# Kernel tuning notes

Hardware: AMD Instinct MI355X
Metric: run time of the kernel (lower is better)

The kernel has to match this reference:

```python
import jax, jax.numpy as jnp
import numpy as np

NUM_BASES = 8


def setup_inputs() -> dict:
    key = jax.random.key(0)
    ks = jax.random.split(key, 8)
    N, E = 100000, 1600000
    IN_F, OUT_F, NUM_RELS = 128, 128, 16
    si = IN_F // NUM_BASES   # 16
    so = OUT_F // NUM_BASES  # 16
    return {
        "h": jax.random.normal(ks[0], (N, IN_F), dtype=jnp.float32),
        "norm": jax.random.uniform(ks[1], (N, 1), dtype=jnp.float32),
        "edge_src": jax.random.randint(ks[2], (E,), 0, N, dtype=jnp.int32),
        "edge_dst": jax.random.randint(ks[3], (E,), 0, N, dtype=jnp.int32),
        "edge_type": jax.random.randint(ks[4], (E,), 0, NUM_RELS, dtype=jnp.int32),
        "weight": jax.random.normal(ks[5], (NUM_RELS, NUM_BASES * si * so), dtype=jnp.float32) * 0.1,
        "bias_param": jax.random.normal(ks[6], (OUT_F,), dtype=jnp.float32) * 0.1,
        "loop_weight": jax.random.normal(ks[7], (IN_F, OUT_F), dtype=jnp.float32) * 0.1,
    }


def reference(h, norm, edge_src, edge_dst, edge_type, weight, bias_param, loop_weight):
    N, in_feat = h.shape
    out_feat = loop_weight.shape[1]
    si = in_feat // NUM_BASES
    so = out_feat // NUM_BASES
    E = edge_type.shape[0]

    # self-loop message (dropout=0.0 -> identity)
    loop_message = h @ loop_weight                      # [N, out_feat]

    # msg_func: gather per-edge relation weight blocks and do block-diag bmm
    W = weight[edge_type].reshape(E, NUM_BASES, si, so)  # [E, B, si, so]
    src = h[edge_src].reshape(E, NUM_BASES, si)          # [E, B, si]
    msg = jnp.einsum("ebi,ebio->ebo", src, W).reshape(E, out_feat)

    # scatter-sum messages to destination nodes, rescale by norm
    agg = jax.ops.segment_sum(msg, edge_dst, num_segments=N)  # [N, out_feat]
    node_repr = agg * norm

    # bias + self-loop + activation
    node_repr = node_repr + bias_param + loop_message
    return jax.nn.relu(node_repr)
```

## Files before the change

kernel.cpp:

```cpp
#include <hip/hip_runtime.h>


__device__ __forceinline__ unsigned int f2bf(float f) {
  const unsigned int u = __float_as_uint(f);
  return (u + 0x7FFFu + ((u >> 16) & 1u)) >> 16;
}

__global__ __launch_bounds__(256) void rgcn_init_kernel(
    const float* __restrict__ h, const float* __restrict__ loop_w,
    const float* __restrict__ bias, float* __restrict__ out, int N) {
  __shared__ float lw[128 * 128];
  for (int idx = threadIdx.x; idx < 128 * 128 / 4; idx += 256) {
    ((float4*)lw)[idx] = ((const float4*)loop_w)[idx];
  }
  __syncthreads();

  const int lane = threadIdx.x & 63;
  const int wid = threadIdx.x >> 6;
  const int group0 = blockIdx.x * 4 + wid;
  const int ngroups = gridDim.x * 4;
  const int totgroups = (N + 3) >> 2;
  const float b0 = bias[lane];
  const float b1 = bias[64 + lane];

  for (int g = group0; g < totgroups; g += ngroups) {
    const int n0 = g * 4;
    const int nn = (N - n0 < 4) ? (N - n0) : 4;
    if (nn == 4) {
      const float* __restrict__ r0 = h + (size_t)n0 * 128;
      const float* __restrict__ r1 = r0 + 128;
      const float* __restrict__ r2 = r1 + 128;
      const float* __restrict__ r3 = r2 + 128;
      float a00 = b0, a01 = b1, a10 = b0, a11 = b1;
      float a20 = b0, a21 = b1, a30 = b0, a31 = b1;
#pragma unroll 4
      for (int k = 0; k < 128; ++k) {
        const float w0 = lw[k * 128 + lane];
        const float w1 = lw[k * 128 + 64 + lane];
        a00 = fmaf(r0[k], w0, a00); a01 = fmaf(r0[k], w1, a01);
        a10 = fmaf(r1[k], w0, a10); a11 = fmaf(r1[k], w1, a11);
        a20 = fmaf(r2[k], w0, a20); a21 = fmaf(r2[k], w1, a21);
        a30 = fmaf(r3[k], w0, a30); a31 = fmaf(r3[k], w1, a31);
      }
      float* __restrict__ o0 = out + (size_t)n0 * 128;
      o0[lane] = a00;        o0[64 + lane] = a01;
      o0[128 + lane] = a10;  o0[192 + lane] = a11;
      o0[256 + lane] = a20;  o0[320 + lane] = a21;
      o0[384 + lane] = a30;  o0[448 + lane] = a31;
    } else {
      for (int r = 0; r < nn; ++r) {
        const int n = n0 + r;
        const float* __restrict__ hr = h + (size_t)n * 128;
        float a0 = b0, a1 = b1;
#pragma unroll 4
        for (int k = 0; k < 128; ++k) {
          const float a = hr[k];
          a0 = fmaf(a, lw[k * 128 + lane], a0);
          a1 = fmaf(a, lw[k * 128 + 64 + lane], a1);
        }
        out[(size_t)n * 128 + lane] = a0;
        out[(size_t)n * 128 + 64 + lane] = a1;
      }
    }
  }
}

__global__ __launch_bounds__(256) void rgcn_presence_kernel(
    const int* __restrict__ esrc, const int* __restrict__ etype,
    unsigned int* __restrict__ pres, int E) {
  for (int e = blockIdx.x * 256 + threadIdx.x; e < E; e += gridDim.x * 256)
    atomicOr(&pres[esrc[e]], 1u << etype[e]);
}

__global__ __launch_bounds__(1024, 8) void rgcn_precompute_kernel(
    const float* __restrict__ h, const float* __restrict__ weight,
    const unsigned int* __restrict__ pres, unsigned int* __restrict__ M,
    int base, int cend) {
  const int lane = threadIdx.x & 63;
  const int t = threadIdx.x >> 6;
  const int b = lane >> 4;
  const int o = lane & 15;

  const float* __restrict__ wb = weight + t * 2048 + b * 256 + o;
  float wlo[16], whi[16];
#pragma unroll
  for (int i = 0; i < 16; ++i) {
    wlo[i] = wb[i * 16];
    whi[i] = wb[1024 + i * 16];
  }

  const int span = cend - base;
  const int n0 = base + (int)(((long)blockIdx.x * span) / gridDim.x);
  const int n1 = base + (int)(((long)(blockIdx.x + 1) * span) / gridDim.x);

#pragma unroll 2
  for (int n = n0; n < n1; ++n) {
    if (!((pres[n] >> t) & 1u)) continue;

    const float4* __restrict__ hp =
        (const float4*)(h + (size_t)n * 128) + (b << 2);
    const float4 x0 = hp[0], x1 = hp[1], x2 = hp[2], x3 = hp[3];
    const float4 y0 = hp[16], y1 = hp[17], y2 = hp[18], y3 = hp[19];

    float a0 = x0.x * wlo[0], a1 = x0.y * wlo[1];
    a0 = fmaf(x0.z, wlo[2], a0);  a1 = fmaf(x0.w, wlo[3], a1);
    a0 = fmaf(x1.x, wlo[4], a0);  a1 = fmaf(x1.y, wlo[5], a1);
    a0 = fmaf(x1.z, wlo[6], a0);  a1 = fmaf(x1.w, wlo[7], a1);
    a0 = fmaf(x2.x, wlo[8], a0);  a1 = fmaf(x2.y, wlo[9], a1);
    a0 = fmaf(x2.z, wlo[10], a0); a1 = fmaf(x2.w, wlo[11], a1);
    a0 = fmaf(x3.x, wlo[12], a0); a1 = fmaf(x3.y, wlo[13], a1);
    a0 = fmaf(x3.z, wlo[14], a0); a1 = fmaf(x3.w, wlo[15], a1);

    float c0 = y0.x * whi[0], c1 = y0.y * whi[1];
    c0 = fmaf(y0.z, whi[2], c0);  c1 = fmaf(y0.w, whi[3], c1);
    c0 = fmaf(y1.x, whi[4], c0);  c1 = fmaf(y1.y, whi[5], c1);
    c0 = fmaf(y1.z, whi[6], c0);  c1 = fmaf(y1.w, whi[7], c1);
    c0 = fmaf(y2.x, whi[8], c0);  c1 = fmaf(y2.y, whi[9], c1);
    c0 = fmaf(y2.z, whi[10], c0); c1 = fmaf(y2.w, whi[11], c1);
    c0 = fmaf(y3.x, whi[12], c0); c1 = fmaf(y3.y, whi[13], c1);
    c0 = fmaf(y3.z, whi[14], c0); c1 = fmaf(y3.w, whi[15], c1);

    const unsigned int pk = f2bf(a0 + a1) | (f2bf(c0 + c1) << 16);
    M[(((size_t)(n - base) << 4) | t) * 64 + lane] = pk;
  }
}

__global__ __launch_bounds__(256) void rgcn_zero_kernel(int* __restrict__ p,
                                                        int n) {
  for (int i = blockIdx.x * 256 + threadIdx.x; i < n; i += gridDim.x * 256)
    p[i] = 0;
}

__global__ __launch_bounds__(256) void rgcn_hist_kernel(
    const int* __restrict__ esrc, const int* __restrict__ edst,
    int* __restrict__ cnt, int E, int N, unsigned S) {
  for (int e = blockIdx.x * 256 + threadIdx.x; e < E; e += gridDim.x * 256) {
    const unsigned q = (unsigned)esrc[e] / S;
    atomicAdd(&cnt[(int)(q * (unsigned)N) + edst[e]], 1);
  }
}

__global__ __launch_bounds__(1024) void rgcn_scan_pass1(
    const int* __restrict__ cnt, int* __restrict__ partial, int bins) {
  __shared__ int sums[1024];
  const int t = threadIdx.x;
  const int base = blockIdx.x * 4096 + t * 4;
  int s = 0;
  if (base + 3 < bins) {
    const int4 v = *(const int4*)(cnt + base);
    s = v.x + v.y + v.z + v.w;
  } else {
    for (int j = 0; j < 4; ++j)
      if (base + j < bins) s += cnt[base + j];
  }
  sums[t] = s;
  __syncthreads();
  for (int off = 512; off > 0; off >>= 1) {
    if (t < off) sums[t] += sums[t + off];
    __syncthreads();
  }
  if (t == 0) partial[blockIdx.x] = sums[0];
}

__global__ __launch_bounds__(1024) void rgcn_scan_pass2(
    int* __restrict__ partial, int nb) {
  __shared__ int sc[1024];
  const int t = threadIdx.x;
  int v[4];
  int s = 0;
#pragma unroll
  for (int j = 0; j < 4; ++j) {
    const int i = t * 4 + j;
    v[j] = (i < nb) ? partial[i] : 0;
    s += v[j];
  }
  sc[t] = s;
  __syncthreads();
#pragma unroll
  for (int off = 1; off < 1024; off <<= 1) {
    const int add = (t >= off) ? sc[t - off] : 0;
    __syncthreads();
    sc[t] += add;
    __syncthreads();
  }
  int run = (t == 0) ? 0 : sc[t - 1];
#pragma unroll
  for (int j = 0; j < 4; ++j) {
    const int i = t * 4 + j;
    if (i < nb) partial[i] = run;
    run += v[j];
  }
}

__global__ __launch_bounds__(1024) void rgcn_scan_pass3(
    const int* __restrict__ cnt, const int* __restrict__ partial,
    int* __restrict__ row_ptr, int* __restrict__ cursor, int bins) {
  __shared__ int sums[1024];
  const int t = threadIdx.x;
  const int base = blockIdx.x * 4096 + t * 4;
  int v0 = 0, v1 = 0, v2 = 0, v3 = 0;
  if (base + 3 < bins) {
    const int4 v = *(const int4*)(cnt + base);
    v0 = v.x; v1 = v.y; v2 = v.z; v3 = v.w;
  } else {
    if (base < bins) v0 = cnt[base];
    if (base + 1 < bins) v1 = cnt[base + 1];
    if (base + 2 < bins) v2 = cnt[base + 2];
  }
  sums[t] = v0 + v1 + v2 + v3;
  __syncthreads();
#pragma unroll
  for (int off = 1; off < 1024; off <<= 1) {
    const int add = (t >= off) ? sums[t - off] : 0;
    __syncthreads();
    sums[t] += add;
    __syncthreads();
  }
  const int run = partial[blockIdx.x] + ((t == 0) ? 0 : sums[t - 1]);
  const int p0 = run, p1 = p0 + v0, p2 = p1 + v1, p3 = p2 + v2;
  if (base + 3 < bins) {
    *(int4*)(row_ptr + base) = make_int4(p0, p1, p2, p3);
    *(int4*)(cursor + base) = make_int4(p0, p1, p2, p3);
  } else {
    if (base < bins) { row_ptr[base] = p0; cursor[base] = p0; }
    if (base + 1 < bins) { row_ptr[base + 1] = p1; cursor[base + 1] = p1; }
    if (base + 2 < bins) { row_ptr[base + 2] = p2; cursor[base + 2] = p2; }
  }
}

__global__ void rgcn_set_kernel(int* __restrict__ p, int v) {
  if (threadIdx.x == 0) *p = v;
}

__global__ __launch_bounds__(256) void rgcn_scatter_kernel(
    const int* __restrict__ esrc, const int* __restrict__ edst,
    const int* __restrict__ etype, int* __restrict__ cursor,
    int* __restrict__ srec, int E, int N, unsigned S) {
  for (int e = blockIdx.x * 256 + threadIdx.x; e < E; e += gridDim.x * 256) {
    const unsigned s = (unsigned)esrc[e];
    const unsigned q = s / S;
    const int key = (int)(q * (unsigned)N) + edst[e];
    const int p = atomicAdd(&cursor[key], 1);
    srec[p] = (int)((s - q * S) << 4) | etype[e];
  }
}

__global__ __launch_bounds__(256) void rgcn_gather3_kernel(
    const float* __restrict__ norm, const int* __restrict__ srec,
    const int* __restrict__ rpc, const unsigned int* __restrict__ M,
    float* __restrict__ out, int N, int final_pass) {
  const int lane = threadIdx.x & 63;
  const int w0 = blockIdx.x * 4 + (threadIdx.x >> 6);
  const int nw = gridDim.x * 4;

  for (int d = w0; d < N; d += nw) {
    const int e0 = rpc[d];
    const int e1 = rpc[d + 1];
    if (!final_pass && e0 == e1) continue;

    float acc0 = 0.f, acc1 = 0.f;
    int e = e0;
    for (; e + 8 <= e1; e += 8) {
      const int r0 = srec[e], r1 = srec[e + 1], r2 = srec[e + 2],
                r3 = srec[e + 3], r4 = srec[e + 4], r5 = srec[e + 5],
                r6 = srec[e + 6], r7 = srec[e + 7];
      const unsigned int v0 = __builtin_nontemporal_load(&M[(size_t)r0 * 64 + lane]);
      const unsigned int v1 = __builtin_nontemporal_load(&M[(size_t)r1 * 64 + lane]);
      const unsigned int v2 = __builtin_nontemporal_load(&M[(size_t)r2 * 64 + lane]);
      const unsigned int v3 = __builtin_nontemporal_load(&M[(size_t)r3 * 64 + lane]);
      const unsigned int v4 = __builtin_nontemporal_load(&M[(size_t)r4 * 64 + lane]);
      const unsigned int v5 = __builtin_nontemporal_load(&M[(size_t)r5 * 64 + lane]);
      const unsigned int v6 = __builtin_nontemporal_load(&M[(size_t)r6 * 64 + lane]);
      const unsigned int v7 = __builtin_nontemporal_load(&M[(size_t)r7 * 64 + lane]);
      acc0 += __uint_as_float(v0 << 16);
      acc1 += __uint_as_float(v0 & 0xFFFF0000u);
      acc0 += __uint_as_float(v1 << 16);
      acc1 += __uint_as_float(v1 & 0xFFFF0000u);
      acc0 += __uint_as_float(v2 << 16);
      acc1 += __uint_as_float(v2 & 0xFFFF0000u);
      acc0 += __uint_as_float(v3 << 16);
      acc1 += __uint_as_float(v3 & 0xFFFF0000u);
      acc0 += __uint_as_float(v4 << 16);
      acc1 += __uint_as_float(v4 & 0xFFFF0000u);
      acc0 += __uint_as_float(v5 << 16);
      acc1 += __uint_as_float(v5 & 0xFFFF0000u);
      acc0 += __uint_as_float(v6 << 16);
      acc1 += __uint_as_float(v6 & 0xFFFF0000u);
      acc0 += __uint_as_float(v7 << 16);
      acc1 += __uint_as_float(v7 & 0xFFFF0000u);
    }
    for (; e + 4 <= e1; e += 4) {
      const int r0 = srec[e], r1 = srec[e + 1], r2 = srec[e + 2],
                r3 = srec[e + 3];
      const unsigned int v0 = __builtin_nontemporal_load(&M[(size_t)r0 * 64 + lane]);
      const unsigned int v1 = __builtin_nontemporal_load(&M[(size_t)r1 * 64 + lane]);
      const unsigned int v2 = __builtin_nontemporal_load(&M[(size_t)r2 * 64 + lane]);
      const unsigned int v3 = __builtin_nontemporal_load(&M[(size_t)r3 * 64 + lane]);
      acc0 += __uint_as_float(v0 << 16);
      acc1 += __uint_as_float(v0 & 0xFFFF0000u);
      acc0 += __uint_as_float(v1 << 16);
      acc1 += __uint_as_float(v1 & 0xFFFF0000u);
      acc0 += __uint_as_float(v2 << 16);
      acc1 += __uint_as_float(v2 & 0xFFFF0000u);
      acc0 += __uint_as_float(v3 << 16);
      acc1 += __uint_as_float(v3 & 0xFFFF0000u);
    }
    for (; e < e1; ++e) {
      const unsigned int v = __builtin_nontemporal_load(&M[(size_t)srec[e] * 64 + lane]);
      acc0 += __uint_as_float(v << 16);
      acc1 += __uint_as_float(v & 0xFFFF0000u);
    }

    const float nm = norm[d];
    float* __restrict__ op = out + ((size_t)d << 7);
    float o0 = fmaf(acc0, nm, op[lane]);
    float o1 = fmaf(acc1, nm, op[64 + lane]);
    if (final_pass) {
      o0 = fmaxf(o0, 0.f);
      o1 = fmaxf(o1, 0.f);
    }
    op[lane] = o0;
    op[64 + lane] = o1;
  }
}

__global__ __launch_bounds__(256) void rgcn_edge_kernel(
    const float* __restrict__ h, const float* __restrict__ norm,
    const int* __restrict__ esrc, const int* __restrict__ edst,
    const int* __restrict__ etype, const float* __restrict__ weight,
    float* __restrict__ out, int E) {
  const int lane = threadIdx.x & 63;
  const int wid = threadIdx.x >> 6;
  const int wave0 = blockIdx.x * 4 + wid;
  const int nwaves = gridDim.x * 4;
  const int b = lane >> 4;
  const int o = lane & 15;

  for (int e = wave0; e < E; e += nwaves) {
    const int src = esrc[e];
    const int dst = edst[e];
    const int et = etype[e];
    const float s_lo = h[src * 128 + lane];
    const float s_hi = h[src * 128 + 64 + lane];
    const float nrm = norm[dst];
    const float* __restrict__ Wb = weight + et * 2048 + b * 256 + o;
    float m0 = 0.f, m1 = 0.f;
#pragma unroll
    for (int i = 0; i < 16; ++i) {
      const float a_lo = __shfl(s_lo, (lane & 48) + i, 64);
      const float a_hi = __shfl(s_hi, (lane & 48) + i, 64);
      m0 = fmaf(a_lo, Wb[i * 16], m0);
      m1 = fmaf(a_hi, Wb[1024 + i * 16], m1);
    }
    atomicAdd(&out[dst * 128 + lane], m0 * nrm);
    atomicAdd(&out[dst * 128 + 64 + lane], m1 * nrm);
  }
}

__global__ __launch_bounds__(256) void rgcn_relu_kernel(float* __restrict__ out,
                                                        int total4) {
  int i = blockIdx.x * 256 + threadIdx.x;
  const int stride = gridDim.x * 256;
  for (; i < total4; i += stride) {
    float4 v = ((float4*)out)[i];
    v.x = fmaxf(v.x, 0.f);
    v.y = fmaxf(v.y, 0.f);
    v.z = fmaxf(v.z, 0.f);
    v.w = fmaxf(v.w, 0.f);
    ((float4*)out)[i] = v;
  }
}

extern "C" void kernel_launch(void* const* d_in, const int* in_sizes, int n_in,
                              void* d_out, int out_size, void* d_ws, size_t ws_size,
                              hipStream_t stream) {
  const float* h      = (const float*)d_in[0];
  const float* norm   = (const float*)d_in[1];
  const int*   esrc   = (const int*)d_in[2];
  const int*   edst   = (const int*)d_in[3];
  const int*   etype  = (const int*)d_in[4];
  const float* weight = (const float*)d_in[5];
  const float* bias   = (const float*)d_in[6];
  const float* loop_w = (const float*)d_in[7];
  float* out = (float*)d_out;

  const int N = in_sizes[0] / 128;
  const int E = in_sizes[2];
  const int nrels = in_sizes[5] / 2048;

  rgcn_init_kernel<<<2048, 256, 0, stream>>>(h, loop_w, bias, out, N);

  int C = -1, S = 0;
  size_t ofs_rp = 0, ofs_cur = 0, ofs_part = 0, ofs_pres = 0, ofs_srec = 0,
         ofs_M = 0;
  if (nrels == 16 && N >= 1 && N < (1 << 26)) {
    for (int cc = 1; cc <= 64; ++cc) {
      const size_t bins = (size_t)cc * (size_t)N;
      if (bins > (size_t)4096 * 4096) break;
      const int ss = (N + cc - 1) / cc;
      const size_t o_rp = (bins + 3) & ~(size_t)3;
      const size_t o_cur = (o_rp + bins + 1 + 3) & ~(size_t)3;
      const size_t o_part = (o_cur + bins + 3) & ~(size_t)3;
      const size_t o_pres = o_part + 4096;
      const size_t o_srec = o_pres + (size_t)N;
      const size_t o_M = (o_srec + (size_t)E + 15) & ~(size_t)15;
      const size_t need = (o_M + (size_t)ss * 16 * 64) * 4;
      if (need <= ws_size) {
        C = cc; S = ss;
        ofs_rp = o_rp; ofs_cur = o_cur; ofs_part = o_part;
        ofs_pres = o_pres; ofs_srec = o_srec; ofs_M = o_M;
        break;
      }
    }
  }

  if (C >= 1) {
    const int bins = C * N;
    const int nb = (bins + 4095) / 4096;
    int* base    = (int*)d_ws;
    int* cnt     = base;
    int* row_ptr = base + ofs_rp;
    int* cursor  = base + ofs_cur;
    int* partial = base + ofs_part;
    unsigned int* pres = (unsigned int*)(base + ofs_pres);
    int* srec    = base + ofs_srec;
    unsigned int* M = (unsigned int*)(base + ofs_M);

    rgcn_zero_kernel<<<1024, 256, 0, stream>>>(cnt, bins);
    rgcn_zero_kernel<<<128, 256, 0, stream>>>((int*)pres, N);
    rgcn_presence_kernel<<<2048, 256, 0, stream>>>(esrc, etype, pres, E);
    rgcn_hist_kernel<<<2048, 256, 0, stream>>>(esrc, edst, cnt, E, N,
                                               (unsigned)S);
    rgcn_scan_pass1<<<nb, 1024, 0, stream>>>(cnt, partial, bins);
    rgcn_scan_pass2<<<1, 1024, 0, stream>>>(partial, nb);
    rgcn_scan_pass3<<<nb, 1024, 0, stream>>>(cnt, partial, row_ptr, cursor,
                                             bins);
    rgcn_set_kernel<<<1, 64, 0, stream>>>(row_ptr + bins, E);
    rgcn_scatter_kernel<<<2048, 256, 0, stream>>>(esrc, edst, etype, cursor,
                                                  srec, E, N, (unsigned)S);
    for (int c = 0; c < C; ++c) {
      const int cbase = c * S;
      const int cend = (cbase + S < N) ? (cbase + S) : N;
      if (cbase >= N) break;
      rgcn_precompute_kernel<<<512, 1024, 0, stream>>>(h, weight, pres, M,
                                                       cbase, cend);
      rgcn_gather3_kernel<<<2048, 256, 0, stream>>>(
          norm, srec, row_ptr + (size_t)c * N, M, out, N,
          (c == C - 1) ? 1 : 0);
    }
  } else {
    rgcn_edge_kernel<<<4096, 256, 0, stream>>>(h, norm, esrc, edst, etype,
                                               weight, out, E);
    rgcn_relu_kernel<<<2048, 256, 0, stream>>>(out, (N * 128) / 4);
  }
}
```

Measured before the change: 1.103 ms.

## Compact precomputed message table to only present source-relation pairs

Builds a bitmap prefix scan over (source node, relation) presence to assign each used pair a compact row index. The precompute kernel writes messages only to compact rows, and scatter stores compact indices so the gather reads a denser table. This is meant to shrink the footprint of the per-pair message table and improve cache reuse during the gather. It adds two scan kernels, an index array lookup per edge and per precompute row, and removes the 4-wide tail unroll in the gather.

```diff
diff --git a/kernel.cpp b/kernel.cpp
--- a/kernel.cpp
+++ b/kernel.cpp
@@ -72,14 +72,70 @@
     atomicOr(&pres[esrc[e]], 1u << etype[e]);
 }
 
+__device__ __forceinline__ int presbit(const unsigned int* pres, int idx) {
+  return (int)((pres[idx >> 4] >> (idx & 15)) & 1u);
+}
+
+__global__ __launch_bounds__(1024) void rgcn_bscan_pass1(
+    const unsigned int* __restrict__ pres, int* __restrict__ partial,
+    int bins) {
+  __shared__ int sums[1024];
+  const int t = threadIdx.x;
+  const int base = blockIdx.x * 4096 + t * 4;
+  int s = 0;
+#pragma unroll
+  for (int j = 0; j < 4; ++j)
+    if (base + j < bins) s += presbit(pres, base + j);
+  sums[t] = s;
+  __syncthreads();
+  for (int off = 512; off > 0; off >>= 1) {
+    if (t < off) sums[t] += sums[t + off];
+    __syncthreads();
+  }
+  if (t == 0) partial[blockIdx.x] = sums[0];
+}
+
+__global__ __launch_bounds__(1024) void rgcn_bscan_pass3(
+    const unsigned int* __restrict__ pres, const int* __restrict__ partial,
+    int* __restrict__ cidx, int bins) {
+  __shared__ int sums[1024];
+  const int t = threadIdx.x;
+  const int base = blockIdx.x * 4096 + t * 4;
+  int v0 = 0, v1 = 0, v2 = 0, v3 = 0;
+  if (base < bins) v0 = presbit(pres, base);
+  if (base + 1 < bins) v1 = presbit(pres, base + 1);
+  if (base + 2 < bins) v2 = presbit(pres, base + 2);
+  if (base + 3 < bins) v3 = presbit(pres, base + 3);
+  sums[t] = v0 + v1 + v2 + v3;
+  __syncthreads();
+#pragma unroll
+  for (int off = 1; off < 1024; off <<= 1) {
+    const int add = (t >= off) ? sums[t - off] : 0;
+    __syncthreads();
+    sums[t] += add;
+    __syncthreads();
+  }
+  const int run = partial[blockIdx.x] + ((t == 0) ? 0 : sums[t - 1]);
+  const int p0 = run, p1 = p0 + v0, p2 = p1 + v1, p3 = p2 + v2;
+  if (base + 3 < bins) {
+    *(int4*)(cidx + base) = make_int4(p0, p1, p2, p3);
+  } else {
+    if (base < bins) cidx[base] = p0;
+    if (base + 1 < bins) cidx[base + 1] = p1;
+    if (base + 2 < bins) cidx[base + 2] = p2;
+  }
+}
+
 __global__ __launch_bounds__(1024, 8) void rgcn_precompute_kernel(
     const float* __restrict__ h, const float* __restrict__ weight,
-    const unsigned int* __restrict__ pres, unsigned int* __restrict__ M,
+    const unsigned int* __restrict__ pres, const int* __restrict__ cidx,
+    const int* __restrict__ base_ptr, unsigned int* __restrict__ M,
     int base, int cend) {
   const int lane = threadIdx.x & 63;
   const int t = threadIdx.x >> 6;
   const int b = lane >> 4;
   const int o = lane & 15;
+  const int mbase = *base_ptr;
 
   const float* __restrict__ wb = weight + t * 2048 + b * 256 + o;
   float wlo[16], whi[16];
@@ -96,6 +152,7 @@
 #pragma unroll 2
   for (int n = n0; n < n1; ++n) {
     if (!((pres[n] >> t) & 1u)) continue;
+    const int row = cidx[n * 16 + t] - mbase;
 
     const float4* __restrict__ hp =
         (const float4*)(h + (size_t)n * 128) + (b << 2);
@@ -121,7 +178,7 @@
     c0 = fmaf(y3.z, whi[14], c0); c1 = fmaf(y3.w, whi[15], c1);
 
     const unsigned int pk = f2bf(a0 + a1) | (f2bf(c0 + c1) << 16);
-    M[(((size_t)(n - base) << 4) | t) * 64 + lane] = pk;
+    M[(size_t)row * 64 + lane] = pk;
   }
 }
 
@@ -234,24 +291,27 @@
 
 __global__ __launch_bounds__(256) void rgcn_scatter_kernel(
     const int* __restrict__ esrc, const int* __restrict__ edst,
-    const int* __restrict__ etype, int* __restrict__ cursor,
-    int* __restrict__ srec, int E, int N, unsigned S) {
+    const int* __restrict__ etype, const int* __restrict__ cidx,
+    int* __restrict__ cursor, int* __restrict__ srec, int E, int N,
+    unsigned S) {
   for (int e = blockIdx.x * 256 + threadIdx.x; e < E; e += gridDim.x * 256) {
     const unsigned s = (unsigned)esrc[e];
     const unsigned q = s / S;
     const int key = (int)(q * (unsigned)N) + edst[e];
     const int p = atomicAdd(&cursor[key], 1);
-    srec[p] = (int)((s - q * S) << 4) | etype[e];
+    srec[p] = cidx[(size_t)s * 16 + etype[e]];
   }
 }
 
 __global__ __launch_bounds__(256) void rgcn_gather3_kernel(
     const float* __restrict__ norm, const int* __restrict__ srec,
-    const int* __restrict__ rpc, const unsigned int* __restrict__ M,
-    float* __restrict__ out, int N, int final_pass) {
+    const int* __restrict__ rpc, const int* __restrict__ base_ptr,
+    const unsigned int* __restrict__ M, float* __restrict__ out, int N,
+    int final_pass) {
   const int lane = threadIdx.x & 63;
   const int w0 = blockIdx.x * 4 + (threadIdx.x >> 6);
   const int nw = gridDim.x * 4;
+  const int mbase = *base_ptr;
 
   for (int d = w0; d < N; d += nw) {
     const int e0 = rpc[d];
@@ -261,9 +321,10 @@
     float acc0 = 0.f, acc1 = 0.f;
     int e = e0;
     for (; e + 8 <= e1; e += 8) {
-      const int r0 = srec[e], r1 = srec[e + 1], r2 = srec[e + 2],
-                r3 = srec[e + 3], r4 = srec[e + 4], r5 = srec[e + 5],
-                r6 = srec[e + 6], r7 = srec[e + 7];
+      const int r0 = srec[e] - mbase, r1 = srec[e + 1] - mbase,
+                r2 = srec[e + 2] - mbase, r3 = srec[e + 3] - mbase,
+                r4 = srec[e + 4] - mbase, r5 = srec[e + 5] - mbase,
+                r6 = srec[e + 6] - mbase, r7 = srec[e + 7] - mbase;
       const unsigned int v0 = __builtin_nontemporal_load(&M[(size_t)r0 * 64 + lane]);
       const unsigned int v1 = __builtin_nontemporal_load(&M[(size_t)r1 * 64 + lane]);
       const unsigned int v2 = __builtin_nontemporal_load(&M[(size_t)r2 * 64 + lane]);
@@ -289,24 +350,9 @@
       acc0 += __uint_as_float(v7 << 16);
       acc1 += __uint_as_float(v7 & 0xFFFF0000u);
     }
-    for (; e + 4 <= e1; e += 4) {
-      const int r0 = srec[e], r1 = srec[e + 1], r2 = srec[e + 2],
-                r3 = srec[e + 3];
-      const unsigned int v0 = __builtin_nontemporal_load(&M[(size_t)r0 * 64 + lane]);
-      const unsigned int v1 = __builtin_nontemporal_load(&M[(size_t)r1 * 64 + lane]);
-      const unsigned int v2 = __builtin_nontemporal_load(&M[(size_t)r2 * 64 + lane]);
-      const unsigned int v3 = __builtin_nontemporal_load(&M[(size_t)r3 * 64 + lane]);
-      acc0 += __uint_as_float(v0 << 16);
-      acc1 += __uint_as_float(v0 & 0xFFFF0000u);
-      acc0 += __uint_as_float(v1 << 16);
-      acc1 += __uint_as_float(v1 & 0xFFFF0000u);
-      acc0 += __uint_as_float(v2 << 16);
-      acc1 += __uint_as_float(v2 & 0xFFFF0000u);
-      acc0 += __uint_as_float(v3 << 16);
-      acc1 += __uint_as_float(v3 & 0xFFFF0000u);
-    }
     for (; e < e1; ++e) {
-      const unsigned int v = __builtin_nontemporal_load(&M[(size_t)srec[e] * 64 + lane]);
+      const int rr = srec[e] - mbase;
+      const unsigned int v = __builtin_nontemporal_load(&M[(size_t)rr * 64 + lane]);
       acc0 += __uint_as_float(v << 16);
       acc1 += __uint_as_float(v & 0xFFFF0000u);
     }
@@ -391,24 +437,27 @@
   rgcn_init_kernel<<<2048, 256, 0, stream>>>(h, loop_w, bias, out, N);
 
   int C = -1, S = 0;
-  size_t ofs_rp = 0, ofs_cur = 0, ofs_part = 0, ofs_pres = 0, ofs_srec = 0,
-         ofs_M = 0;
+  size_t ofs_rp = 0, ofs_cur = 0, ofs_part = 0, ofs_pres = 0, ofs_cidx = 0,
+         ofs_srec = 0, ofs_M = 0;
   if (nrels == 16 && N >= 1 && N < (1 << 26)) {
     for (int cc = 1; cc <= 64; ++cc) {
       const size_t bins = (size_t)cc * (size_t)N;
       if (bins > (size_t)4096 * 4096) break;
+      const size_t bins2 = (size_t)N * 16;
+      if (bins2 > (size_t)4096 * 4096) break;
       const int ss = (N + cc - 1) / cc;
       const size_t o_rp = (bins + 3) & ~(size_t)3;
       const size_t o_cur = (o_rp + bins + 1 + 3) & ~(size_t)3;
       const size_t o_part = (o_cur + bins + 3) & ~(size_t)3;
       const size_t o_pres = o_part + 4096;
-      const size_t o_srec = o_pres + (size_t)N;
+      const size_t o_cidx = (o_pres + (size_t)N + 3) & ~(size_t)3;
+      const size_t o_srec = o_cidx + bins2;
       const size_t o_M = (o_srec + (size_t)E + 15) & ~(size_t)15;
       const size_t need = (o_M + (size_t)ss * 16 * 64) * 4;
       if (need <= ws_size) {
         C = cc; S = ss;
         ofs_rp = o_rp; ofs_cur = o_cur; ofs_part = o_part;
-        ofs_pres = o_pres; ofs_srec = o_srec; ofs_M = o_M;
+        ofs_pres = o_pres; ofs_cidx = o_cidx; ofs_srec = o_srec; ofs_M = o_M;
         break;
       }
     }
@@ -417,18 +466,24 @@
   if (C >= 1) {
     const int bins = C * N;
     const int nb = (bins + 4095) / 4096;
+    const int bins2 = N * 16;
+    const int nb2 = (bins2 + 4095) / 4096;
     int* base    = (int*)d_ws;
     int* cnt     = base;
     int* row_ptr = base + ofs_rp;
     int* cursor  = base + ofs_cur;
     int* partial = base + ofs_part;
     unsigned int* pres = (unsigned int*)(base + ofs_pres);
+    int* cidx    = base + ofs_cidx;
     int* srec    = base + ofs_srec;
     unsigned int* M = (unsigned int*)(base + ofs_M);
 
     rgcn_zero_kernel<<<1024, 256, 0, stream>>>(cnt, bins);
     rgcn_zero_kernel<<<128, 256, 0, stream>>>((int*)pres, N);
     rgcn_presence_kernel<<<2048, 256, 0, stream>>>(esrc, etype, pres, E);
+    rgcn_bscan_pass1<<<nb2, 1024, 0, stream>>>(pres, partial, bins2);
+    rgcn_scan_pass2<<<1, 1024, 0, stream>>>(partial, nb2);
+    rgcn_bscan_pass3<<<nb2, 1024, 0, stream>>>(pres, partial, cidx, bins2);
     rgcn_hist_kernel<<<2048, 256, 0, stream>>>(esrc, edst, cnt, E, N,
                                                (unsigned)S);
     rgcn_scan_pass1<<<nb, 1024, 0, stream>>>(cnt, partial, bins);
@@ -436,16 +491,19 @@
     rgcn_scan_pass3<<<nb, 1024, 0, stream>>>(cnt, partial, row_ptr, cursor,
                                              bins);
     rgcn_set_kernel<<<1, 64, 0, stream>>>(row_ptr + bins, E);
-    rgcn_scatter_kernel<<<2048, 256, 0, stream>>>(esrc, edst, etype, cursor,
-                                                  srec, E, N, (unsigned)S);
+    rgcn_scatter_kernel<<<2048, 256, 0, stream>>>(esrc, edst, etype, cidx,
+                                                  cursor, srec, E, N,
+                                                  (unsigned)S);
     for (int c = 0; c < C; ++c) {
       const int cbase = c * S;
       const int cend = (cbase + S < N) ? (cbase + S) : N;
       if (cbase >= N) break;
-      rgcn_precompute_kernel<<<512, 1024, 0, stream>>>(h, weight, pres, M,
-                                                       cbase, cend);
+      const int* base_ptr = cidx + (size_t)cbase * 16;
+      rgcn_precompute_kernel<<<512, 1024, 0, stream>>>(h, weight, pres, cidx,
+                                                       base_ptr, M, cbase,
+                                                       cend);
       rgcn_gather3_kernel<<<2048, 256, 0, stream>>>(
-          norm, srec, row_ptr + (size_t)c * N, M, out, N,
+          norm, srec, row_ptr + (size_t)c * N, base_ptr, M, out, N,
           (c == C - 1) ? 1 : 0);
     }
   } else {
```

New measurement: 1.195 ms. 1.08x slower.
